# Optimization experiments

Hardware: AMD Instinct MI355X
Metric: run time of the kernel (lower is better)

## Reference

```python
import jax, jax.numpy as jnp
import numpy as np

N_NODES = 30000
N_EDGES = 480000
B_PAIRS = 4096


def _lin(key, fan_in, fan_out):
    k1, k2 = jax.random.split(key)
    s = 1.0 / np.sqrt(fan_in)
    W = jax.random.uniform(k1, (fan_in, fan_out), minval=-s, maxval=s, dtype=jnp.float32)
    b = jax.random.uniform(k2, (fan_out,), minval=-s, maxval=s, dtype=jnp.float32)
    return W, b


def setup_inputs() -> dict:
    key = jax.random.key(0)
    ks = jax.random.split(key, 20)
    inp = {}
    inp["cid"] = jax.random.normal(ks[0], (N_NODES, 881), dtype=jnp.float32)
    inp["link_edge"] = jax.random.randint(ks[1], (2, N_EDGES), 0, N_NODES, dtype=jnp.int64)
    inp["i1"] = jax.random.randint(ks[2], (B_PAIRS,), 0, N_NODES, dtype=jnp.int64)
    inp["i2"] = jax.random.randint(ks[3], (B_PAIRS,), 0, N_NODES, dtype=jnp.int64)
    inp["soft_thr"] = jnp.array(0.01, jnp.float32)
    inp["bb_fc2_W"], inp["bb_fc2_b"] = _lin(ks[4], 881, 881)
    inp["bb_fc3_W"], inp["bb_fc3_b"] = _lin(ks[5], 881, 256)
    inp["gcn1_W"], inp["gcn1_b"] = _lin(ks[6], 256, 256)
    inp["gcn2_W"], inp["gcn2_b"] = _lin(ks[7], 256, 256)
    inp["gcn3_W"], inp["gcn3_b"] = _lin(ks[8], 256, 256)
    inp["gcn4_W"], inp["gcn4_b"] = _lin(ks[9], 256, 128)
    inp["gcn5_W"], inp["gcn5_b"] = _lin(ks[10], 128, 128)
    inp["fc1_W"], inp["fc1_b"] = _lin(ks[11], 256, 1024)
    inp["fc2_W"], inp["fc2_b"] = _lin(ks[12], 1024, 256)
    inp["fc3_W"], inp["fc3_b"] = _lin(ks[13], 256, 64)
    inp["out_W"], inp["out_b"] = _lin(ks[14], 64, 2)
    return inp


def _forward(cid, link_edge, i1, i2, soft_thr,
             bb_fc2_W, bb_fc2_b, bb_fc3_W, bb_fc3_b,
             gcn1_W, gcn1_b, gcn2_W, gcn2_b, gcn3_W, gcn3_b,
             gcn4_W, gcn4_b, gcn5_W, gcn5_b,
             fc1_W, fc1_b, fc2_W, fc2_b, fc3_W, fc3_b, out_W, out_b):
    N = cid.shape[0]
    # --- BasicBlock1 (eval mode, dropout off everywhere) ---
    x = jax.nn.relu(cid @ bb_fc2_W + bb_fc2_b)
    x = jnp.sign(x) * jax.nn.relu(jnp.abs(x) - soft_thr)  # soft threshold
    x = jax.nn.relu(x @ bb_fc3_W + bb_fc3_b)              # [N, 256]

    # --- GCN normalization (PyG GCNConv: add self-loops, sym norm) ---
    loop = jnp.arange(N, dtype=link_edge.dtype)
    src = jnp.concatenate([link_edge[0], loop])
    dst = jnp.concatenate([link_edge[1], loop])
    deg = jax.ops.segment_sum(jnp.ones_like(dst, dtype=jnp.float32), dst, num_segments=N)
    dinv = jnp.where(deg > 0, jax.lax.rsqrt(deg), 0.0)
    enorm = (dinv[src] * dinv[dst])[:, None]  # [E+N, 1]

    def gcn(h, W, b):
        h = h @ W                                            # [N, F_out]
        msg = h[src] * enorm                                 # gather + scale
        return jax.ops.segment_sum(msg, dst, num_segments=N) + b

    h = jax.nn.elu(gcn(x, gcn1_W, gcn1_b))
    h = jax.nn.elu(gcn(h, gcn2_W, gcn2_b))
    h = jax.nn.elu(gcn(h, gcn3_W, gcn3_b))
    h = jax.nn.elu(gcn(h, gcn4_W, gcn4_b))
    h = jax.nn.elu(gcn(h, gcn5_W, gcn5_b))                   # [N, 128]

    # --- pair readout ---
    xc = jnp.concatenate([h[i1], h[i2]], axis=1)             # [B, 256]
    norm = jnp.maximum(jnp.linalg.norm(xc, axis=1, keepdims=True), 1e-12)
    xc = xc / norm                                           # F.normalize(p=2, dim=1)
    xc = jax.nn.relu(xc @ fc1_W + fc1_b)
    xc = jax.nn.relu(xc @ fc2_W + fc2_b)
    xc = jax.nn.relu(xc @ fc3_W + fc3_b)
    return xc @ out_W + out_b                                # [B, 2]


def reference(cid, link_edge, i1, i2, soft_thr,
              bb_fc2_W, bb_fc2_b, bb_fc3_W, bb_fc3_b,
              gcn1_W, gcn1_b, gcn2_W, gcn2_b, gcn3_W, gcn3_b,
              gcn4_W, gcn4_b, gcn5_W, gcn5_b,
              fc1_W, fc1_b, fc2_W, fc2_b, fc3_W, fc3_b, out_W, out_b):
    return _forward(cid, link_edge, i1, i2, soft_thr,
                    bb_fc2_W, bb_fc2_b, bb_fc3_W, bb_fc3_b,
                    gcn1_W, gcn1_b, gcn2_W, gcn2_b, gcn3_W, gcn3_b,
                    gcn4_W, gcn4_b, gcn5_W, gcn5_b,
                    fc1_W, fc1_b, fc2_W, fc2_b, fc3_W, fc3_b, out_W, out_b)
```

## Files before the change

### kernel.cpp

```cpp
#include <hip/hip_runtime.h>
#include <hip/hip_bf16.h>
#include <math.h>


#define NNODES 30000
#define NEDGES 480000
#define NPAIRS 4096

typedef __attribute__((ext_vector_type(8))) short short8;
typedef __attribute__((ext_vector_type(4))) short short4v;
typedef __attribute__((ext_vector_type(2))) short short2v;
typedef __attribute__((ext_vector_type(4))) float f32x4;
typedef __attribute__((ext_vector_type(2))) float f32x2;
typedef unsigned short u16;

__device__ __forceinline__ u16 f2bf(float x) {
    union { float f; unsigned u; } v; v.f = x;
    unsigned u = v.u;
    return (u16)((u + 0x7FFFu + ((u >> 16) & 1u)) >> 16);
}
__device__ __forceinline__ float bf2f(u16 h) {
    union { float f; unsigned u; } v; v.u = ((unsigned)h) << 16;
    return v.f;
}

__device__ __forceinline__ void gll16(const u16* g, u16* l) {
    __builtin_amdgcn_global_load_lds(
        (const __attribute__((address_space(1))) unsigned int*)g,
        (__attribute__((address_space(3))) unsigned int*)l, 16, 0, 0);
}


__global__ void k_count(const int* __restrict__ dst, unsigned* __restrict__ cnt, int E) {
    int e = blockIdx.x * blockDim.x + threadIdx.x;
    if (e < E) atomicAdd(&cnt[dst[e]], 1u);
}

__global__ void k_dinv(const unsigned* __restrict__ cnt, float* __restrict__ dinv, int N) {
    int n = blockIdx.x * blockDim.x + threadIdx.x;
    if (n < N) {
        float deg = (float)(cnt[n] + 1u);
        dinv[n] = 1.0f / sqrtf(deg);
    }
}

__global__ void k_scan(const unsigned* __restrict__ cnt, unsigned* __restrict__ rowptr, int N) {
    __shared__ unsigned buf[1024];
    __shared__ unsigned carry_s;
    const int tid = threadIdx.x;
    if (tid == 0) { carry_s = 0; rowptr[0] = 0; }
    __syncthreads();
    for (int base = 0; base < N; base += 1024) {
        int i = base + tid;
        unsigned v = (i < N) ? cnt[i] : 0u;
        buf[tid] = v;
        __syncthreads();
        for (int off = 1; off < 1024; off <<= 1) {
            unsigned t = (tid >= off) ? buf[tid - off] : 0u;
            __syncthreads();
            buf[tid] += t;
            __syncthreads();
        }
        unsigned c = carry_s;
        if (i < N) rowptr[i + 1] = c + buf[tid];
        __syncthreads();
        if (tid == 1023) carry_s = c + buf[1023];
        __syncthreads();
    }
}

__global__ void k_fill(const int* __restrict__ src, const int* __restrict__ dst,
                       const unsigned* __restrict__ rowptr, unsigned* __restrict__ cursor,
                       int* __restrict__ colsrc, int E) {
    int e = blockIdx.x * blockDim.x + threadIdx.x;
    if (e < E) {
        int d = dst[e];
        unsigned p = atomicAdd(&cursor[d], 1u);
        colsrc[rowptr[d] + p] = src[e];
    }
}


__global__ void k_wconv(const float* __restrict__ W, u16* __restrict__ Th,
                        u16* __restrict__ Tl, int K, int N, int Kp, int Np) {
    int idx = blockIdx.x * blockDim.x + threadIdx.x;
    if (idx >= Np * Kp) return;
    int n = idx / Kp, k = idx - n * Kp;
    float v = (n < N && k < K) ? W[(size_t)k * N + n] : 0.f;
    u16 h = f2bf(v);
    Th[idx] = h;
    Tl[idx] = f2bf(v - bf2f(h));
}

__global__ void k_aconv(const float* __restrict__ A, u16* __restrict__ Hh,
                        u16* __restrict__ Hl) {
    int idx = blockIdx.x * blockDim.x + threadIdx.x;
    if (idx >= NNODES * 896) return;
    int row = idx / 896, col = idx - row * 896;
    float v = (col < 881) ? A[(size_t)row * 881 + col] : 0.f;
    u16 h = f2bf(v);
    Hh[idx] = h;
    Hl[idx] = f2bf(v - bf2f(h));
}


template <int ASRC, int EPI, int OUTM>
__global__ __launch_bounds__(256) void k_mgemm(
    const float* __restrict__ Af, int ldAf, int Ktrue,
    const u16* __restrict__ Ahi, const u16* __restrict__ Alo, int ldA,
    const u16* __restrict__ Bhi, const u16* __restrict__ Blo, int ldB,
    const float* __restrict__ bias, const float* __restrict__ thrp,
    const float* __restrict__ rowscale,
    float* __restrict__ Cf, u16* __restrict__ Chi, u16* __restrict__ Clo,
    int ldC, int M, int Ntrue, int K, int gy) {
    __shared__ alignas(16) u16 Ah[128 * 32];
    __shared__ alignas(16) u16 Al[128 * 32];
    __shared__ alignas(16) u16 Bh[128 * 32];
    __shared__ alignas(16) u16 Bl[128 * 32];
    const int t = threadIdx.x;
    const int lane = t & 63, w = t >> 6;
    const int wr = w >> 1, wc = w & 1;
    const int r16 = lane & 15, kg = lane >> 4;
    const int nwg = gridDim.x;
    const int q = nwg >> 3, r = nwg & 7;
    const int xcd = blockIdx.x & 7, pos = blockIdx.x >> 3;
    const int wg = (xcd < r ? xcd * (q + 1) : r * (q + 1) + (xcd - r) * q) + pos;
    const int bx = wg / gy, by = wg - bx * gy;
    const int bm = bx * 128, bn = by * 128;
    const int srow = (w << 5) + (lane >> 2);
    const int k8 = (lane & 3) << 3;
    const int lb = w << 11;
    f32x4 acc[4][4] = {};

    const int arow = t >> 1, kq = (t & 1) << 4;
    int gmA = bm + arow; if (gmA >= M) gmA = M - 1;
    const float* aBase = (ASRC == 0) ? (Af + (size_t)gmA * ldAf) : nullptr;
    float aR[16];

    auto LOADA = [&](int k0) {
#pragma unroll
        for (int j = 0; j < 16; ++j) aR[j] = aBase[k0 + kq + j];
    };
    auto WRITEA = [&](int k0) {
        short8 hv0, lv0, hv1, lv1;
#pragma unroll
        for (int j = 0; j < 8; ++j) {
            float v = (k0 + kq + j < Ktrue) ? aR[j] : 0.f;
            u16 hh = f2bf(v);
            hv0[j] = (short)hh;
            lv0[j] = (short)f2bf(v - bf2f(hh));
        }
#pragma unroll
        for (int j = 0; j < 8; ++j) {
            float v = (k0 + kq + 8 + j < Ktrue) ? aR[8 + j] : 0.f;
            u16 hh = f2bf(v);
            hv1[j] = (short)hh;
            lv1[j] = (short)f2bf(v - bf2f(hh));
        }
        const int wa = arow * 32 + kq;
        *(short8*)&Ah[wa] = hv0;  *(short8*)&Ah[wa + 8] = hv1;
        *(short8*)&Al[wa] = lv0;  *(short8*)&Al[wa + 8] = lv1;
    };

    if (ASRC == 0) LOADA(0);
    for (int k0 = 0; k0 < K; k0 += 32) {
        gll16(Bhi + (size_t)(bn + srow) * ldB + k0 + k8, (u16*)((char*)Bh + lb));
        gll16(Bhi + (size_t)(bn + srow + 16) * ldB + k0 + k8, (u16*)((char*)Bh + lb + 1024));
        gll16(Blo + (size_t)(bn + srow) * ldB + k0 + k8, (u16*)((char*)Bl + lb));
        gll16(Blo + (size_t)(bn + srow + 16) * ldB + k0 + k8, (u16*)((char*)Bl + lb + 1024));
        if (ASRC == 0) {
            WRITEA(k0);
        } else {
            gll16(Ahi + (size_t)(bm + srow) * ldA + k0 + k8, (u16*)((char*)Ah + lb));
            gll16(Ahi + (size_t)(bm + srow + 16) * ldA + k0 + k8, (u16*)((char*)Ah + lb + 1024));
            gll16(Alo + (size_t)(bm + srow) * ldA + k0 + k8, (u16*)((char*)Al + lb));
            gll16(Alo + (size_t)(bm + srow + 16) * ldA + k0 + k8, (u16*)((char*)Al + lb + 1024));
        }
        __syncthreads();
        if (ASRC == 0 && k0 + 32 < K) LOADA(k0 + 32);
        short8 fah[4], fal[4];
#pragma unroll
        for (int mi = 0; mi < 4; ++mi) {
            const int off = (wr * 64 + mi * 16 + r16) * 32 + kg * 8;
            fah[mi] = *(const short8*)&Ah[off];
            fal[mi] = *(const short8*)&Al[off];
        }
#pragma unroll
        for (int ni = 0; ni < 4; ++ni) {
            const int off = (wc * 64 + ni * 16 + r16) * 32 + kg * 8;
            const short8 fbh = *(const short8*)&Bh[off];
            const short8 fbl = *(const short8*)&Bl[off];
#pragma unroll
            for (int mi = 0; mi < 4; ++mi) {
                acc[mi][ni] = __builtin_amdgcn_mfma_f32_16x16x32_bf16(fah[mi], fbh, acc[mi][ni], 0, 0, 0);
                acc[mi][ni] = __builtin_amdgcn_mfma_f32_16x16x32_bf16(fal[mi], fbh, acc[mi][ni], 0, 0, 0);
                acc[mi][ni] = __builtin_amdgcn_mfma_f32_16x16x32_bf16(fah[mi], fbl, acc[mi][ni], 0, 0, 0);
            }
        }
        __syncthreads();
    }

    const float thr = (EPI == 2) ? *thrp : 0.f;
#pragma unroll
    for (int mi = 0; mi < 4; ++mi) {
#pragma unroll
        for (int i = 0; i < 4; ++i) {
            const int m = bm + wr * 64 + mi * 16 + kg * 4 + i;
            if (m >= M) continue;
            const float rs = (OUTM == 2) ? rowscale[m] : 1.f;
#pragma unroll
            for (int ni = 0; ni < 4; ++ni) {
                const int n = bn + wc * 64 + ni * 16 + r16;
                float z = acc[mi][ni][i];
                if (EPI >= 1) {
                    z += (n < Ntrue) ? bias[n] : 0.f;
                    z = (EPI == 1) ? fmaxf(z, 0.f) : fmaxf(z - thr, 0.f);
                }
                if (OUTM == 0) {
                    if (n < Ntrue) Cf[(size_t)m * ldC + n] = z;
                } else if (OUTM == 2) {
                    if (n < Ntrue) Cf[(size_t)m * ldC + n] = z * rs;
                } else {
                    if (n < ldC) {
                        if (n >= Ntrue) z = 0.f;
                        u16 h = f2bf(z);
                        size_t o = (size_t)m * ldC + n;
                        Chi[o] = h;
                        Clo[o] = f2bf(z - bf2f(h));
                    }
                }
            }
        }
    }
}


template <int FV, int WB>
__global__ __launch_bounds__(256) void k_agg(
    const float* __restrict__ hWs, const float* __restrict__ dinv,
    const unsigned* __restrict__ rowptr, const int* __restrict__ colsrc,
    const float* __restrict__ bias, float* __restrict__ outf,
    u16* __restrict__ oh, u16* __restrict__ ol, int N) {
    const int wave = threadIdx.x >> 6;
    const int lane = threadIdx.x & 63;
    const int n = blockIdx.x * 4 + wave;
    if (n >= N) return;
    const int F = FV * 64;
    const int fb = lane * FV;
    const float* __restrict__ hbase = hWs + fb;
    float acc[FV];
    {
        if (FV == 4) {
            const f32x4 v = *(const f32x4*)(hbase + (size_t)n * F);
#pragma unroll
            for (int j = 0; j < FV; ++j) acc[j] = v[j];
        } else {
            const f32x2 v = *(const f32x2*)(hbase + (size_t)n * F);
#pragma unroll
            for (int j = 0; j < FV; ++j) acc[j] = v[j];
        }
    }
    unsigned idx = rowptr[n];
    const unsigned end = rowptr[n + 1];
    for (; idx + 4 <= end; idx += 4) {
        int s0 = colsrc[idx], s1 = colsrc[idx + 1], s2 = colsrc[idx + 2], s3 = colsrc[idx + 3];
        if (FV == 4) {
            const f32x4 v0 = *(const f32x4*)(hbase + (size_t)s0 * F);
            const f32x4 v1 = *(const f32x4*)(hbase + (size_t)s1 * F);
            const f32x4 v2 = *(const f32x4*)(hbase + (size_t)s2 * F);
            const f32x4 v3 = *(const f32x4*)(hbase + (size_t)s3 * F);
#pragma unroll
            for (int j = 0; j < FV; ++j) acc[j] += (v0[j] + v1[j]) + (v2[j] + v3[j]);
        } else {
            const f32x2 v0 = *(const f32x2*)(hbase + (size_t)s0 * F);
            const f32x2 v1 = *(const f32x2*)(hbase + (size_t)s1 * F);
            const f32x2 v2 = *(const f32x2*)(hbase + (size_t)s2 * F);
            const f32x2 v3 = *(const f32x2*)(hbase + (size_t)s3 * F);
#pragma unroll
            for (int j = 0; j < FV; ++j) acc[j] += (v0[j] + v1[j]) + (v2[j] + v3[j]);
        }
    }
    for (; idx < end; ++idx) {
        int s0 = colsrc[idx];
        if (FV == 4) {
            const f32x4 v0 = *(const f32x4*)(hbase + (size_t)s0 * F);
#pragma unroll
            for (int j = 0; j < FV; ++j) acc[j] += v0[j];
        } else {
            const f32x2 v0 = *(const f32x2*)(hbase + (size_t)s0 * F);
#pragma unroll
            for (int j = 0; j < FV; ++j) acc[j] += v0[j];
        }
    }
    const float dn = dinv[n];
    float z[FV];
#pragma unroll
    for (int j = 0; j < FV; ++j) {
        float zz = dn * acc[j] + bias[fb + j];
        z[j] = (zz > 0.f) ? zz : expm1f(zz);
    }
    if (WB) {
        if (FV == 4) {
            short4v hv, lv;
#pragma unroll
            for (int j = 0; j < 4; ++j) {
                u16 h = f2bf(z[j]);
                hv[j] = (short)h;
                lv[j] = (short)f2bf(z[j] - bf2f(h));
            }
            *(short4v*)(oh + (size_t)n * F + fb) = hv;
            *(short4v*)(ol + (size_t)n * F + fb) = lv;
        } else {
            short2v hv, lv;
#pragma unroll
            for (int j = 0; j < 2; ++j) {
                u16 h = f2bf(z[j]);
                hv[j] = (short)h;
                lv[j] = (short)f2bf(z[j] - bf2f(h));
            }
            *(short2v*)(oh + (size_t)n * F + fb) = hv;
            *(short2v*)(ol + (size_t)n * F + fb) = lv;
        }
    } else {
        if (FV == 4) {
            f32x4 v;
#pragma unroll
            for (int j = 0; j < 4; ++j) v[j] = z[j];
            *(f32x4*)(outf + (size_t)n * F + fb) = v;
        } else {
            f32x2 v;
#pragma unroll
            for (int j = 0; j < 2; ++j) v[j] = z[j];
            *(f32x2*)(outf + (size_t)n * F + fb) = v;
        }
    }
}


__global__ __launch_bounds__(256) void k_pairs(
    const float* __restrict__ h, const int* __restrict__ i1, const int* __restrict__ i2,
    u16* __restrict__ xh, u16* __restrict__ xl, int B) {
    const int wave = threadIdx.x >> 6;
    const int lane = threadIdx.x & 63;
    const int p = blockIdx.x * 4 + wave;
    if (p >= B) return;
    const int a = i1[p], b = i2[p];
    float v0 = h[(size_t)a * 128 + lane];
    float v1 = h[(size_t)a * 128 + 64 + lane];
    float v2 = h[(size_t)b * 128 + lane];
    float v3 = h[(size_t)b * 128 + 64 + lane];
    float ss = v0 * v0 + v1 * v1 + v2 * v2 + v3 * v3;
#pragma unroll
    for (int o = 32; o > 0; o >>= 1) ss += __shfl_xor(ss, o, 64);
    float scale = 1.0f / fmaxf(sqrtf(ss), 1e-12f);
    size_t o = (size_t)p * 256;
    float vv[4] = {v0 * scale, v1 * scale, v2 * scale, v3 * scale};
#pragma unroll
    for (int j = 0; j < 4; ++j) {
        u16 hh = f2bf(vv[j]);
        xh[o + j * 64 + lane] = hh;
        xl[o + j * 64 + lane] = f2bf(vv[j] - bf2f(hh));
    }
}

__global__ __launch_bounds__(256) void k_out(
    const float* __restrict__ x, const float* __restrict__ W, const float* __restrict__ b,
    float* __restrict__ out, int B) {
    const int wave = threadIdx.x >> 6;
    const int lane = threadIdx.x & 63;
    const int p = blockIdx.x * 4 + wave;
    if (p >= B) return;
    float v = x[(size_t)p * 64 + lane];
    float s0 = v * W[lane * 2 + 0];
    float s1 = v * W[lane * 2 + 1];
#pragma unroll
    for (int o = 32; o > 0; o >>= 1) {
        s0 += __shfl_xor(s0, o, 64);
        s1 += __shfl_xor(s1, o, 64);
    }
    if (lane == 0) {
        out[p * 2 + 0] = s0 + b[0];
        out[p * 2 + 1] = s1 + b[1];
    }
}


extern "C" void kernel_launch(void* const* d_in, const int* in_sizes, int n_in,
                              void* d_out, int out_size, void* d_ws, size_t ws_size,
                              hipStream_t stream) {
    const float* cid = (const float*)d_in[0];
    const int* le   = (const int*)d_in[1];
    const int* i1   = (const int*)d_in[2];
    const int* i2   = (const int*)d_in[3];
    const float* thr = (const float*)d_in[4];
    const float* W2 = (const float*)d_in[5];  const float* b2 = (const float*)d_in[6];
    const float* W3 = (const float*)d_in[7];  const float* b3 = (const float*)d_in[8];
    const float* gW[5] = {(const float*)d_in[9],  (const float*)d_in[11], (const float*)d_in[13],
                          (const float*)d_in[15], (const float*)d_in[17]};
    const float* gB[5] = {(const float*)d_in[10], (const float*)d_in[12], (const float*)d_in[14],
                          (const float*)d_in[16], (const float*)d_in[18]};
    const float* fc1W = (const float*)d_in[19]; const float* fc1b = (const float*)d_in[20];
    const float* fc2W = (const float*)d_in[21]; const float* fc2b = (const float*)d_in[22];
    const float* fc3W = (const float*)d_in[23]; const float* fc3b = (const float*)d_in[24];
    const float* oW   = (const float*)d_in[25]; const float* ob   = (const float*)d_in[26];

    const int N = NNODES, E = NEDGES, B = NPAIRS;
    char* ws = (char*)d_ws;
    const bool big = ws_size >= 230000000ull;

    unsigned* cnt    = (unsigned*)(ws + 0);
    unsigned* cursor = (unsigned*)(ws + 120064);
    unsigned* rowptr = (unsigned*)(ws + 240128);
    int*      colsrc = (int*)     (ws + 360192);
    float*    dinv   = (float*)   (ws + 2280192);
    u16* W2th = (u16*)(ws + 2400256);  u16* W2tl = (u16*)(ws + 4005888);
    u16* W3th = (u16*)(ws + 5611520);  u16* W3tl = (u16*)(ws + 6070272);
    u16* g1h  = (u16*)(ws + 6529024);  u16* g1l  = (u16*)(ws + 6660096);
    u16* g2h  = (u16*)(ws + 6791168);  u16* g2l  = (u16*)(ws + 6922240);
    u16* g3h  = (u16*)(ws + 7053312);  u16* g3l  = (u16*)(ws + 7184384);
    u16* g4h  = (u16*)(ws + 7315456);  u16* g4l  = (u16*)(ws + 7380992);
    u16* g5h  = (u16*)(ws + 7446528);  u16* g5l  = (u16*)(ws + 7479296);
    u16* f1h  = (u16*)(ws + 7512064);  u16* f1l  = (u16*)(ws + 8036352);
    u16* f2h  = (u16*)(ws + 8560640);  u16* f2l  = (u16*)(ws + 9084928);
    u16* f3h  = (u16*)(ws + 9609216);  u16* f3l  = (u16*)(ws + 9674752);

    u16 *cidh = nullptr, *cidl = nullptr;
    u16 *x1h, *x1l, *x2h, *x2l, *hAh, *hAl, *xch, *xcl, *t1h, *t1l, *t2h, *t2l;
    float *hWs, *hfin, *t3;
    if (big) {
        const size_t CB = 9740288;
        const size_t XB = CB + 2ull * 53903360;
        cidh = (u16*)(ws + CB);
        cidl = (u16*)(ws + CB + 53903360);
        x1h  = (u16*)(ws + XB);
        x1l  = (u16*)(ws + XB + 53903360);
        x2h  = (u16*)(ws + CB);
        x2l  = (u16*)(ws + CB + 15400960);
        hWs  = (float*)(ws + CB + 30801920);
        hfin = (float*)(ws + CB + 61603840);
        xch  = (u16*)(ws + CB + 76963840);
        xcl  = (u16*)(ws + CB + 79060992);
        t1h  = (u16*)(ws + CB + 81158144);
        t1l  = (u16*)(ws + CB + 89546752);
        t2h  = (u16*)(ws + CB + 97935360);
        t2l  = (u16*)(ws + CB + 100032512);
        t3   = (float*)(ws + CB + 102129664);
        hAh  = (u16*)(ws + XB);
        hAl  = (u16*)(ws + XB + 15400960);
    } else {
        const size_t X1 = 40542208;
        x2h = (u16*)(ws + 9740288);
        x2l = (u16*)(ws + 25141248);
        x1h = (u16*)(ws + X1);
        x1l = (u16*)(ws + X1 + 53903360);
        hWs  = (float*)(ws + X1);
        hAh  = (u16*)  (ws + X1 + 30801920);
        hAl  = (u16*)  (ws + X1 + 46202880);
        hfin = (float*)(ws + X1 + 61603840);
        xch  = (u16*)  (ws + X1 + 76963840);
        xcl  = (u16*)  (ws + X1 + 79060992);
        t1h  = (u16*)  (ws + X1 + 81158144);
        t1l  = (u16*)  (ws + X1 + 89546752);
        t2h  = (u16*)  (ws + X1 + 97935360);
        t2l  = (u16*)  (ws + X1 + 100032512);
        t3   = (float*)(ws + X1 + 102129664);
    }

    hipMemsetAsync(cnt, 0, N * sizeof(unsigned), stream);
    hipMemsetAsync(cursor, 0, N * sizeof(unsigned), stream);
    k_count<<<(E + 255) / 256, 256, 0, stream>>>(le + E, cnt, E);
    k_dinv<<<(N + 255) / 256, 256, 0, stream>>>(cnt, dinv, N);
    k_scan<<<1, 1024, 0, stream>>>(cnt, rowptr, N);
    k_fill<<<(E + 255) / 256, 256, 0, stream>>>(le, le + E, rowptr, cursor, colsrc, E);

    k_wconv<<<3136, 256, 0, stream>>>(W2, W2th, W2tl, 881, 881, 896, 896);
    k_wconv<<<896, 256, 0, stream>>>(W3, W3th, W3tl, 881, 256, 896, 256);
    k_wconv<<<256, 256, 0, stream>>>(gW[0], g1h, g1l, 256, 256, 256, 256);
    k_wconv<<<256, 256, 0, stream>>>(gW[1], g2h, g2l, 256, 256, 256, 256);
    k_wconv<<<256, 256, 0, stream>>>(gW[2], g3h, g3l, 256, 256, 256, 256);
    k_wconv<<<128, 256, 0, stream>>>(gW[3], g4h, g4l, 256, 128, 256, 128);
    k_wconv<<<64, 256, 0, stream>>>(gW[4], g5h, g5l, 128, 128, 128, 128);
    k_wconv<<<1024, 256, 0, stream>>>(fc1W, f1h, f1l, 256, 1024, 256, 1024);
    k_wconv<<<1024, 256, 0, stream>>>(fc2W, f2h, f2l, 1024, 256, 1024, 256);
    k_wconv<<<128, 256, 0, stream>>>(fc3W, f3h, f3l, 256, 64, 256, 128);

    const int MB = (N + 127) / 128;

    if (big) {
        k_aconv<<<(NNODES * 896 + 255) / 256, 256, 0, stream>>>(cid, cidh, cidl);
        k_mgemm<1, 2, 1><<<MB * 7, 256, 0, stream>>>(
            nullptr, 0, 0, cidh, cidl, 896, W2th, W2tl, 896, b2, thr, nullptr,
            nullptr, x1h, x1l, 896, N, 881, 896, 7);
    } else {
        k_mgemm<0, 2, 1><<<MB * 7, 256, 0, stream>>>(
            cid, 881, 881, nullptr, nullptr, 0, W2th, W2tl, 896, b2, thr, nullptr,
            nullptr, x1h, x1l, 896, N, 881, 896, 7);
    }
    k_mgemm<1, 1, 1><<<MB * 2, 256, 0, stream>>>(
        nullptr, 0, 0, x1h, x1l, 896, W3th, W3tl, 896, b3, nullptr, nullptr,
        nullptr, x2h, x2l, 256, N, 256, 896, 2);

    const u16* wh[5] = {g1h, g2h, g3h, g4h, g5h};
    const u16* wl[5] = {g1l, g2l, g3l, g4l, g5l};
    const int fin[5]  = {256, 256, 256, 256, 128};
    const int fout[5] = {256, 256, 256, 128, 128};
    u16* curh = x2h;  u16* curl = x2l;
    for (int l = 0; l < 5; ++l) {
        const int gy = fout[l] / 128;
        k_mgemm<1, 0, 2><<<MB * gy, 256, 0, stream>>>(
            nullptr, 0, 0, curh, curl, fin[l], wh[l], wl[l], fin[l], nullptr, nullptr, dinv,
            hWs, nullptr, nullptr, fout[l], N, fout[l], fin[l], gy);
        if (l == 4) {
            k_agg<2, 0><<<(N + 3) / 4, 256, 0, stream>>>(hWs, dinv, rowptr, colsrc, gB[l],
                                                         hfin, nullptr, nullptr, N);
        } else if (fout[l] == 256) {
            u16* oh = (l & 1) ? x2h : hAh;
            u16* ol = (l & 1) ? x2l : hAl;
            k_agg<4, 1><<<(N + 3) / 4, 256, 0, stream>>>(hWs, dinv, rowptr, colsrc, gB[l],
                                                         nullptr, oh, ol, N);
            curh = oh; curl = ol;
        } else {
            k_agg<2, 1><<<(N + 3) / 4, 256, 0, stream>>>(hWs, dinv, rowptr, colsrc, gB[l],
                                                         nullptr, x2h, x2l, N);
            curh = x2h; curl = x2l;
        }
    }

    k_pairs<<<(B + 3) / 4, 256, 0, stream>>>(hfin, i1, i2, xch, xcl, B);
    k_mgemm<1, 1, 1><<<32 * 8, 256, 0, stream>>>(
        nullptr, 0, 0, xch, xcl, 256, f1h, f1l, 256, fc1b, nullptr, nullptr,
        nullptr, t1h, t1l, 1024, B, 1024, 256, 8);
    k_mgemm<1, 1, 1><<<32 * 2, 256, 0, stream>>>(
        nullptr, 0, 0, t1h, t1l, 1024, f2h, f2l, 1024, fc2b, nullptr, nullptr,
        nullptr, t2h, t2l, 256, B, 256, 1024, 2);
    k_mgemm<1, 1, 0><<<32 * 1, 256, 0, stream>>>(
        nullptr, 0, 0, t2h, t2l, 256, f3h, f3l, 256, fc3b, nullptr, nullptr,
        t3, nullptr, nullptr, 64, B, 64, 256, 1);
    k_out<<<(B + 3) / 4, 256, 0, stream>>>(t3, oW, ob, (float*)d_out, B);
}
```

Baseline: 1.174 ms.

## Slice GCN aggregation by feature chunk, parallelize scan, batch weight conversions

The GCN aggregation now splits each node's features into 32-float slices, with consecutive blocks covering different slices of the same node group. Each half-wave handles one node's slice with scalar loads, which raises parallelism and is meant to improve cache locality of the gathered rows. The single-block prefix scan becomes a three-kernel block scan, and the ten weight-conversion launches are merged into one kernel driven by a job table. The trade-offs are narrower, less vectorized memory accesses and extra launches for the scan.

```diff
diff --git a/kernel.cpp b/kernel.cpp
--- a/kernel.cpp
+++ b/kernel.cpp
@@ -8,10 +8,7 @@
 #define NPAIRS 4096
 
 typedef __attribute__((ext_vector_type(8))) short short8;
-typedef __attribute__((ext_vector_type(4))) short short4v;
-typedef __attribute__((ext_vector_type(2))) short short2v;
 typedef __attribute__((ext_vector_type(4))) float f32x4;
-typedef __attribute__((ext_vector_type(2))) float f32x2;
 typedef unsigned short u16;
 
 __device__ __forceinline__ u16 f2bf(float x) {
@@ -44,29 +41,35 @@
     }
 }
 
-__global__ void k_scan(const unsigned* __restrict__ cnt, unsigned* __restrict__ rowptr, int N) {
-    __shared__ unsigned buf[1024];
-    __shared__ unsigned carry_s;
-    const int tid = threadIdx.x;
-    if (tid == 0) { carry_s = 0; rowptr[0] = 0; }
+__global__ void k_scan1(const unsigned* __restrict__ cnt, unsigned* __restrict__ loc,
+                        unsigned* __restrict__ part, int N) {
+    __shared__ unsigned buf[256];
+    int i = blockIdx.x * 256 + threadIdx.x;
+    unsigned v = (i < N) ? cnt[i] : 0u;
+    buf[threadIdx.x] = v;
     __syncthreads();
-    for (int base = 0; base < N; base += 1024) {
-        int i = base + tid;
-        unsigned v = (i < N) ? cnt[i] : 0u;
-        buf[tid] = v;
+    for (int off = 1; off < 256; off <<= 1) {
+        unsigned t = (threadIdx.x >= (unsigned)off) ? buf[threadIdx.x - off] : 0u;
         __syncthreads();
-        for (int off = 1; off < 1024; off <<= 1) {
-            unsigned t = (tid >= off) ? buf[tid - off] : 0u;
-            __syncthreads();
-            buf[tid] += t;
-            __syncthreads();
-        }
-        unsigned c = carry_s;
-        if (i < N) rowptr[i + 1] = c + buf[tid];
+        buf[threadIdx.x] += t;
         __syncthreads();
-        if (tid == 1023) carry_s = c + buf[1023];
-        __syncthreads();
-    }
+    }
+    if (i < N) loc[i] = buf[threadIdx.x];
+    if (threadIdx.x == 255) part[blockIdx.x] = buf[255];
+}
+
+__global__ void k_scan2(unsigned* __restrict__ part, int nb) {
+    if (threadIdx.x == 0 && blockIdx.x == 0) {
+        unsigned s = 0;
+        for (int i = 0; i < nb; ++i) { unsigned t = part[i]; part[i] = s; s += t; }
+    }
+}
+
+__global__ void k_scan3(const unsigned* __restrict__ loc, const unsigned* __restrict__ part,
+                        unsigned* __restrict__ rowptr, int N) {
+    int i = blockIdx.x * 256 + threadIdx.x;
+    if (i < N) rowptr[i + 1] = loc[i] + part[blockIdx.x];
+    if (i == 0) rowptr[0] = 0;
 }
 
 __global__ void k_fill(const int* __restrict__ src, const int* __restrict__ dst,
@@ -81,15 +84,23 @@
 }
 
 
-__global__ void k_wconv(const float* __restrict__ W, u16* __restrict__ Th,
-                        u16* __restrict__ Tl, int K, int N, int Kp, int Np) {
-    int idx = blockIdx.x * blockDim.x + threadIdx.x;
-    if (idx >= Np * Kp) return;
-    int n = idx / Kp, k = idx - n * Kp;
-    float v = (n < N && k < K) ? W[(size_t)k * N + n] : 0.f;
+struct WJob { const float* W; u16* Th; u16* Tl; int K, N, Kp, Np, endBlk; };
+struct WJobs { WJob j[10]; };
+
+__global__ void k_wconv_all(WJobs js) {
+    const int b = blockIdx.x;
+    WJob jb = js.j[0];
+    int blk0 = 0;
+#pragma unroll
+    for (int t = 1; t < 10; ++t)
+        if (b >= js.j[t - 1].endBlk) { jb = js.j[t]; blk0 = js.j[t - 1].endBlk; }
+    int idx = (b - blk0) * 256 + threadIdx.x;
+    if (idx >= jb.Np * jb.Kp) return;
+    int n = idx / jb.Kp, k = idx - n * jb.Kp;
+    float v = (n < jb.N && k < jb.K) ? jb.W[(size_t)k * jb.N + n] : 0.f;
     u16 h = f2bf(v);
-    Th[idx] = h;
-    Tl[idx] = f2bf(v - bf2f(h));
+    jb.Th[idx] = h;
+    jb.Tl[idx] = f2bf(v - bf2f(h));
 }
 
 __global__ void k_aconv(const float* __restrict__ A, u16* __restrict__ Hh,
@@ -235,104 +246,44 @@
 }
 
 
-template <int FV, int WB>
-__global__ __launch_bounds__(256) void k_agg(
+template <int NS, int WB>
+__global__ __launch_bounds__(256) void k_aggs(
     const float* __restrict__ hWs, const float* __restrict__ dinv,
     const unsigned* __restrict__ rowptr, const int* __restrict__ colsrc,
     const float* __restrict__ bias, float* __restrict__ outf,
     u16* __restrict__ oh, u16* __restrict__ ol, int N) {
+    const int F = NS * 32;
+    const int m = blockIdx.x & 7;
+    const int g = blockIdx.x >> 3;
+    const int slice = (NS == 8) ? m : (m & 3);
+    const int nbase = (NS == 8) ? (g << 3) : ((g << 4) + ((m >> 2) << 3));
     const int wave = threadIdx.x >> 6;
-    const int lane = threadIdx.x & 63;
-    const int n = blockIdx.x * 4 + wave;
+    const int half = (threadIdx.x >> 5) & 1;
+    const int ln = threadIdx.x & 31;
+    const int n = nbase + (wave << 1) + half;
     if (n >= N) return;
-    const int F = FV * 64;
-    const int fb = lane * FV;
-    const float* __restrict__ hbase = hWs + fb;
-    float acc[FV];
-    {
-        if (FV == 4) {
-            const f32x4 v = *(const f32x4*)(hbase + (size_t)n * F);
-#pragma unroll
-            for (int j = 0; j < FV; ++j) acc[j] = v[j];
-        } else {
-            const f32x2 v = *(const f32x2*)(hbase + (size_t)n * F);
-#pragma unroll
-            for (int j = 0; j < FV; ++j) acc[j] = v[j];
-        }
-    }
+    const int fb = (slice << 5) + ln;
+    const float* __restrict__ hb = hWs + fb;
+    float acc = hb[(size_t)n * F];
     unsigned idx = rowptr[n];
     const unsigned end = rowptr[n + 1];
     for (; idx + 4 <= end; idx += 4) {
-        int s0 = colsrc[idx], s1 = colsrc[idx + 1], s2 = colsrc[idx + 2], s3 = colsrc[idx + 3];
-        if (FV == 4) {
-            const f32x4 v0 = *(const f32x4*)(hbase + (size_t)s0 * F);
-            const f32x4 v1 = *(const f32x4*)(hbase + (size_t)s1 * F);
-            const f32x4 v2 = *(const f32x4*)(hbase + (size_t)s2 * F);
-            const f32x4 v3 = *(const f32x4*)(hbase + (size_t)s3 * F);
-#pragma unroll
-            for (int j = 0; j < FV; ++j) acc[j] += (v0[j] + v1[j]) + (v2[j] + v3[j]);
-        } else {
-            const f32x2 v0 = *(const f32x2*)(hbase + (size_t)s0 * F);
-            const f32x2 v1 = *(const f32x2*)(hbase + (size_t)s1 * F);
-            const f32x2 v2 = *(const f32x2*)(hbase + (size_t)s2 * F);
-            const f32x2 v3 = *(const f32x2*)(hbase + (size_t)s3 * F);
-#pragma unroll
-            for (int j = 0; j < FV; ++j) acc[j] += (v0[j] + v1[j]) + (v2[j] + v3[j]);
-        }
-    }
-    for (; idx < end; ++idx) {
-        int s0 = colsrc[idx];
-        if (FV == 4) {
-            const f32x4 v0 = *(const f32x4*)(hbase + (size_t)s0 * F);
-#pragma unroll
-            for (int j = 0; j < FV; ++j) acc[j] += v0[j];
-        } else {
-            const f32x2 v0 = *(const f32x2*)(hbase + (size_t)s0 * F);
-#pragma unroll
-            for (int j = 0; j < FV; ++j) acc[j] += v0[j];
-        }
-    }
-    const float dn = dinv[n];
-    float z[FV];
-#pragma unroll
-    for (int j = 0; j < FV; ++j) {
-        float zz = dn * acc[j] + bias[fb + j];
-        z[j] = (zz > 0.f) ? zz : expm1f(zz);
-    }
+        int s0 = colsrc[idx], s1 = colsrc[idx + 1];
+        int s2 = colsrc[idx + 2], s3 = colsrc[idx + 3];
+        float a0 = hb[(size_t)s0 * F], a1 = hb[(size_t)s1 * F];
+        float a2 = hb[(size_t)s2 * F], a3 = hb[(size_t)s3 * F];
+        acc += (a0 + a1) + (a2 + a3);
+    }
+    for (; idx < end; ++idx) acc += hb[(size_t)colsrc[idx] * F];
+    float z = dinv[n] * acc + bias[fb];
+    z = (z > 0.f) ? z : expm1f(z);
+    const size_t o = (size_t)n * F + fb;
     if (WB) {
-        if (FV == 4) {
-            short4v hv, lv;
-#pragma unroll
-            for (int j = 0; j < 4; ++j) {
-                u16 h = f2bf(z[j]);
-                hv[j] = (short)h;
-                lv[j] = (short)f2bf(z[j] - bf2f(h));
-            }
-            *(short4v*)(oh + (size_t)n * F + fb) = hv;
-            *(short4v*)(ol + (size_t)n * F + fb) = lv;
-        } else {
-            short2v hv, lv;
-#pragma unroll
-            for (int j = 0; j < 2; ++j) {
-                u16 h = f2bf(z[j]);
-                hv[j] = (short)h;
-                lv[j] = (short)f2bf(z[j] - bf2f(h));
-            }
-            *(short2v*)(oh + (size_t)n * F + fb) = hv;
-            *(short2v*)(ol + (size_t)n * F + fb) = lv;
-        }
+        u16 h = f2bf(z);
+        oh[o] = h;
+        ol[o] = f2bf(z - bf2f(h));
     } else {
-        if (FV == 4) {
-            f32x4 v;
-#pragma unroll
-            for (int j = 0; j < 4; ++j) v[j] = z[j];
-            *(f32x4*)(outf + (size_t)n * F + fb) = v;
-        } else {
-            f32x2 v;
-#pragma unroll
-            for (int j = 0; j < 2; ++j) v[j] = z[j];
-            *(f32x2*)(outf + (size_t)n * F + fb) = v;
-        }
+        outf[o] = z;
     }
 }
 
@@ -412,6 +363,8 @@
     unsigned* cursor = (unsigned*)(ws + 120064);
     unsigned* rowptr = (unsigned*)(ws + 240128);
     int*      colsrc = (int*)     (ws + 360192);
+    unsigned* loc    = (unsigned*)(ws + 360192);
+    unsigned* part   = (unsigned*)(ws + 360192 + 122880);
     float*    dinv   = (float*)   (ws + 2280192);
     u16* W2th = (u16*)(ws + 2400256);  u16* W2tl = (u16*)(ws + 4005888);
     u16* W3th = (u16*)(ws + 5611520);  u16* W3tl = (u16*)(ws + 6070272);
@@ -470,19 +423,31 @@
     hipMemsetAsync(cursor, 0, N * sizeof(unsigned), stream);
     k_count<<<(E + 255) / 256, 256, 0, stream>>>(le + E, cnt, E);
     k_dinv<<<(N + 255) / 256, 256, 0, stream>>>(cnt, dinv, N);
-    k_scan<<<1, 1024, 0, stream>>>(cnt, rowptr, N);
+    const int NB = (N + 255) / 256;
+    k_scan1<<<NB, 256, 0, stream>>>(cnt, loc, part, N);
+    k_scan2<<<1, 64, 0, stream>>>(part, NB);
+    k_scan3<<<NB, 256, 0, stream>>>(loc, part, rowptr, N);
     k_fill<<<(E + 255) / 256, 256, 0, stream>>>(le, le + E, rowptr, cursor, colsrc, E);
 
-    k_wconv<<<3136, 256, 0, stream>>>(W2, W2th, W2tl, 881, 881, 896, 896);
-    k_wconv<<<896, 256, 0, stream>>>(W3, W3th, W3tl, 881, 256, 896, 256);
-    k_wconv<<<256, 256, 0, stream>>>(gW[0], g1h, g1l, 256, 256, 256, 256);
-    k_wconv<<<256, 256, 0, stream>>>(gW[1], g2h, g2l, 256, 256, 256, 256);
-    k_wconv<<<256, 256, 0, stream>>>(gW[2], g3h, g3l, 256, 256, 256, 256);
-    k_wconv<<<128, 256, 0, stream>>>(gW[3], g4h, g4l, 256, 128, 256, 128);
-    k_wconv<<<64, 256, 0, stream>>>(gW[4], g5h, g5l, 128, 128, 128, 128);
-    k_wconv<<<1024, 256, 0, stream>>>(fc1W, f1h, f1l, 256, 1024, 256, 1024);
-    k_wconv<<<1024, 256, 0, stream>>>(fc2W, f2h, f2l, 1024, 256, 1024, 256);
-    k_wconv<<<128, 256, 0, stream>>>(fc3W, f3h, f3l, 256, 64, 256, 128);
+    {
+        WJobs js;
+        int e = 0;
+        auto set = [&](int i, const float* W, u16* Th, u16* Tl, int K, int Nn, int Kp, int Np) {
+            e += (Np * Kp) / 256;
+            js.j[i] = WJob{W, Th, Tl, K, Nn, Kp, Np, e};
+        };
+        set(0, W2, W2th, W2tl, 881, 881, 896, 896);
+        set(1, W3, W3th, W3tl, 881, 256, 896, 256);
+        set(2, gW[0], g1h, g1l, 256, 256, 256, 256);
+        set(3, gW[1], g2h, g2l, 256, 256, 256, 256);
+        set(4, gW[2], g3h, g3l, 256, 256, 256, 256);
+        set(5, gW[3], g4h, g4l, 256, 128, 256, 128);
+        set(6, gW[4], g5h, g5l, 128, 128, 128, 128);
+        set(7, fc1W, f1h, f1l, 256, 1024, 256, 1024);
+        set(8, fc2W, f2h, f2l, 1024, 256, 1024, 256);
+        set(9, fc3W, f3h, f3l, 256, 64, 256, 128);
+        k_wconv_all<<<e, 256, 0, stream>>>(js);
+    }
 
     const int MB = (N + 127) / 128;
 
@@ -511,17 +476,17 @@
             nullptr, 0, 0, curh, curl, fin[l], wh[l], wl[l], fin[l], nullptr, nullptr, dinv,
             hWs, nullptr, nullptr, fout[l], N, fout[l], fin[l], gy);
         if (l == 4) {
-            k_agg<2, 0><<<(N + 3) / 4, 256, 0, stream>>>(hWs, dinv, rowptr, colsrc, gB[l],
-                                                         hfin, nullptr, nullptr, N);
+            k_aggs<4, 0><<<8 * ((N + 15) / 16), 256, 0, stream>>>(
+                hWs, dinv, rowptr, colsrc, gB[l], hfin, nullptr, nullptr, N);
         } else if (fout[l] == 256) {
             u16* oh = (l & 1) ? x2h : hAh;
             u16* ol = (l & 1) ? x2l : hAl;
-            k_agg<4, 1><<<(N + 3) / 4, 256, 0, stream>>>(hWs, dinv, rowptr, colsrc, gB[l],
-                                                         nullptr, oh, ol, N);
+            k_aggs<8, 1><<<8 * ((N + 7) / 8), 256, 0, stream>>>(
+                hWs, dinv, rowptr, colsrc, gB[l], nullptr, oh, ol, N);
             curh = oh; curl = ol;
         } else {
-            k_agg<2, 1><<<(N + 3) / 4, 256, 0, stream>>>(hWs, dinv, rowptr, colsrc, gB[l],
-                                                         nullptr, x2h, x2l, N);
+            k_aggs<4, 1><<<8 * ((N + 15) / 16), 256, 0, stream>>>(
+                hWs, dinv, rowptr, colsrc, gB[l], nullptr, x2h, x2l, N);
             curh = x2h; curl = x2l;
         }
     }
```

Result: no change. 1.179 ms (+0.4%).
